# Optimization experiments

Measured on AMD Instinct MI355X. Metric: run time of the kernel, lower is better.

Reference implementation:

```python
import jax, jax.numpy as jnp
import numpy as np

B, T = 8192, 26
V, E, H, L = 23, 100, 128, 64  # vocab, emb dim, GRU hidden, latent; LSTM hidden = E


def setup_inputs() -> dict:
    key = jax.random.key(0)
    ks = jax.random.split(key, 16)
    rn = lambda k, shape, scale=0.1: (jax.random.normal(k, shape, jnp.float32) * scale)
    emb = rn(ks[0], (V, E)).at[0].set(0.0)  # padding_idx=0 row zeroed
    return {
        "z": jax.random.normal(ks[1], (B, L), jnp.float32),
        "x_in": jax.random.randint(ks[2], (B, T), 0, V),
        "emb": emb,
        "fc_z_w": rn(ks[3], (H, L)), "fc_z_b": rn(ks[4], (H,)),
        "gru_wih": rn(ks[5], (3 * H, E)), "gru_whh": rn(ks[6], (3 * H, H)),
        "gru_bih": rn(ks[7], (3 * H,)), "gru_bhh": rn(ks[8], (3 * H,)),
        "lstm_wih": rn(ks[9], (4 * E, H)), "lstm_whh": rn(ks[10], (4 * E, E)),
        "lstm_bih": rn(ks[11], (4 * E,)), "lstm_bhh": rn(ks[12], (4 * E,)),
        "out_w": rn(ks[13], (V, E)), "out_b": rn(ks[14], (V,)),
    }


def _gru(e, h0, Wih, Whh, bih, bhh):
    # e: (B,T,E); precompute input projections for all steps, scan over T.
    xg = jnp.einsum('bti,gi->btg', e, Wih) + bih  # (B,T,3H)

    def step(h, x):
        hg = h @ Whh.T + bhh
        xr, xz, xn = jnp.split(x, 3, axis=-1)
        hr, hz, hn = jnp.split(hg, 3, axis=-1)
        r = jax.nn.sigmoid(xr + hr)
        zg = jax.nn.sigmoid(xz + hz)
        n = jnp.tanh(xn + r * hn)
        h_new = (1.0 - zg) * n + zg * h
        return h_new, h_new

    _, ys = jax.lax.scan(step, h0, jnp.swapaxes(xg, 0, 1))  # (T,B,H)
    return jnp.swapaxes(ys, 0, 1)


def _lstm(x, h0, c0, Wih, Whh, bih, bhh):
    xg = jnp.einsum('bti,gi->btg', x, Wih) + bih  # (B,T,4E)

    def step(hc, xt):
        h, c = hc
        g = xt + h @ Whh.T + bhh
        i, f, gg, o = jnp.split(g, 4, axis=-1)
        c_new = jax.nn.sigmoid(f) * c + jax.nn.sigmoid(i) * jnp.tanh(gg)
        h_new = jax.nn.sigmoid(o) * jnp.tanh(c_new)
        return (h_new, c_new), h_new

    _, ys = jax.lax.scan(step, (h0, c0), jnp.swapaxes(xg, 0, 1))
    return jnp.swapaxes(ys, 0, 1)


def reference(z, x_in, emb, fc_z_w, fc_z_b, gru_wih, gru_whh, gru_bih, gru_bhh,
              lstm_wih, lstm_whh, lstm_bih, lstm_bhh, out_w, out_b):
    h0 = jnp.tanh(z @ fc_z_w.T + fc_z_b)            # (B,H)
    e = emb[x_in]                                    # (B,T,E)
    y = _gru(e, h0, gru_wih, gru_whh, gru_bih, gru_bhh)           # (B,T,H)
    zeros = jnp.zeros((z.shape[0], E), dtype=z.dtype)
    y = _lstm(y, zeros, zeros, lstm_wih, lstm_whh, lstm_bih, lstm_bhh)  # (B,T,E)
    logits = jnp.einsum('bte,ve->btv', y, out_w) + out_b          # (B,T,V)
    return logits
```

## Files before the change

kernel.cpp:

```cpp
#include <hip/hip_runtime.h>
#include <stdint.h>
#include <stddef.h>

#define BB 8192
#define TT 26
#define VV 23
#define EE 100
#define HH 128
#define LL 64

typedef __attribute__((ext_vector_type(8))) short bf16x8;
typedef __attribute__((ext_vector_type(4))) float f32x4;

#define MFMA(a, b, c) __builtin_amdgcn_mfma_f32_16x16x32_bf16((a), (b), (c), 0, 0, 0)

#define OFF_GRUW   0ull
#define OFF_TBL    98304ull
#define OFF_LSTMW  122880ull
#define OFF_OUTW   352256ull
#define OFF_FCZW   360448ull
#define OFF_LBIAS  376832ull

#define L_LW    0
#define L_HF    114688
#define L_LH    131072
#define L_IDX   147456
#define L_TOTAL 148480

__device__ __forceinline__ void force_frag(bf16x8& v) { asm volatile("" : "+v"(v)); }

__device__ __forceinline__ unsigned short f2bf(float f) {
  union { float f; unsigned u; } v; v.f = f;
  unsigned u = v.u;
  return (unsigned short)((u + 0x7FFFu + ((u >> 16) & 1u)) >> 16);
}
__device__ __forceinline__ unsigned short f2bf_fast(float f) {
  union { float f; unsigned u; } v; v.f = f;
  return (unsigned short)((v.u + 0x8000u) >> 16);
}
#define LOG2E 1.4426950408889634f
__device__ __forceinline__ float sigm(float x) {
  return __builtin_amdgcn_rcpf(1.0f + __builtin_amdgcn_exp2f(-x * LOG2E));
}
__device__ __forceinline__ float tanh_(float x) {
  return __builtin_fmaf(-2.0f,
      __builtin_amdgcn_rcpf(1.0f + __builtin_amdgcn_exp2f(x * (2.0f * LOG2E))), 1.0f);
}

__global__ __launch_bounds__(512) void prep_table_kernel(
    const float* __restrict__ emb, const float* __restrict__ gru_wih,
    const float* __restrict__ gru_bih, char* __restrict__ ws)
{
  __shared__ float emb_s[VV * EE];
  __shared__ float wih_s[16 * EE];
  __shared__ float bih_s[16];
  const int tid = threadIdx.x;
  const int ct  = blockIdx.x;
  const int n0  = ct * 16;

  for (int i = tid; i < VV * EE; i += 512) emb_s[i] = emb[i];
  for (int i = tid; i < 16 * EE; i += 512) wih_s[i] = gru_wih[n0 * EE + i];
  if (tid < 16) bih_s[tid] = gru_bih[n0 + tid];
  __syncthreads();

  const int j    = tid & 7;
  const int lane = (tid >> 3) & 63;
  const int n16  = lane & 15;
  const int k    = ((lane >> 4) & 3) * 8 + j;
  float v = 0.0f;
  if (k < VV) {
    const float* ep = emb_s + k * EE;
    const float* wp = wih_s + n16 * EE;
    float s0 = 0.f, s1 = 0.f, s2 = 0.f, s3 = 0.f;
#pragma unroll 5
    for (int m = 0; m < EE; m += 4) {
      s0 += ep[m] * wp[m];         s1 += ep[m + 1] * wp[m + 1];
      s2 += ep[m + 2] * wp[m + 2]; s3 += ep[m + 3] * wp[m + 3];
    }
    v = bih_s[n16] + ((s0 + s1) + (s2 + s3));
  }
  *(unsigned short*)(ws + OFF_TBL + (size_t)(ct * 512 + tid) * 2) = f2bf(v);
}

__global__ __launch_bounds__(256) void prep_main_kernel(
    const float* __restrict__ fc_z_w, const float* __restrict__ gru_whh,
    const float* __restrict__ lstm_wih, const float* __restrict__ lstm_whh,
    const float* __restrict__ lstm_bih, const float* __restrict__ lstm_bhh,
    const float* __restrict__ out_w, char* __restrict__ ws)
{
  int e = blockIdx.x * 256 + threadIdx.x;

  if (e < 49152) {
    int j = e & 7, lane = (e >> 3) & 63, kc = (e >> 9) & 3, ct = e >> 11;
    int n = ct * 16 + (lane & 15);
    int k = kc * 32 + ((lane >> 4) & 3) * 8 + j;
    *(unsigned short*)(ws + OFF_GRUW + (size_t)e * 2) = f2bf(gru_whh[n * HH + k]);
    return;
  }
  e -= 49152;
  if (e < 114688) {
    int j = e & 7, lane = (e >> 3) & 63, kc = (e >> 9) & 7, ct = e >> 12;
    int row = ct * 16 + (lane & 15);
    int g = row / 112, c = row % 112;
    int q = (lane >> 4) & 3;
    float v = 0.0f;
    if (c < EE) {
      if (kc < 4) {
        int k = kc * 32 + q * 8 + j;
        v = lstm_wih[(g * EE + c) * HH + k];
      } else {
        int k = (kc - 4) * 32 + q * 8 + j;
        if (k < EE) v = lstm_whh[(g * EE + c) * EE + k];
      }
    }
    *(unsigned short*)(ws + OFF_LSTMW + (size_t)e * 2) = f2bf(v);
    return;
  }
  e -= 114688;
  if (e < 4096) {
    int j = e & 7, lane = (e >> 3) & 63, kc = (e >> 9) & 3, ct = e >> 11;
    int n = ct * 16 + (lane & 15);
    int k = kc * 32 + ((lane >> 4) & 3) * 8 + j;
    float v = (n < VV && k < EE) ? out_w[n * EE + k] : 0.0f;
    *(unsigned short*)(ws + OFF_OUTW + (size_t)e * 2) = f2bf(v);
    return;
  }
  e -= 4096;
  if (e < 8192) {
    int j = e & 7, lane = (e >> 3) & 63, kc = (e >> 9) & 1, ct = e >> 10;
    int n = ct * 16 + (lane & 15);
    int k = kc * 32 + ((lane >> 4) & 3) * 8 + j;
    *(unsigned short*)(ws + OFF_FCZW + (size_t)e * 2) = f2bf(fc_z_w[n * LL + k]);
    return;
  }
  e -= 8192;
  if (e < 448) {
    int g = e / 112, c = e % 112;
    float v = (c < EE) ? (lstm_bih[g * EE + c] + lstm_bhh[g * EE + c]) : 0.0f;
    *(float*)(ws + OFF_LBIAS + (size_t)e * 4) = v;
  }
}

__global__ __launch_bounds__(1024, 4) void fused_kernel(
    const float* __restrict__ z, const int* __restrict__ x_in,
    const float* __restrict__ fc_z_b, const float* __restrict__ gru_bhh,
    const unsigned short* __restrict__ gruw, const unsigned short* __restrict__ tbl,
    const unsigned short* __restrict__ fczw,
    const unsigned short* __restrict__ lstmw, const float* __restrict__ lbias,
    const float* __restrict__ out_b, const unsigned short* __restrict__ outw,
    float* __restrict__ out)
{
  extern __shared__ char smem[];
  unsigned short* lwlds = (unsigned short*)(smem + L_LW);
  char*           hfrag = smem + L_HF;
  char*           lhbuf = smem + L_LH;
  unsigned char*  idx_lds = (unsigned char*)(smem + L_IDX);

  const int tid  = threadIdx.x;
  const int wv   = tid >> 6;
  const int lane = tid & 63;
  const int l15  = lane & 15;
  const int q    = (lane >> 4) & 3;
  const int blk  = blockIdx.x;

  for (int i = tid; i < 8192; i += 1024)
    ((unsigned short*)lhbuf)[i] = 0;
  for (int f = tid; f < 7168; f += 1024) {
    int frag_i = f >> 6, within = f & 63;
    int ct = frag_i >> 2, kcl = frag_i & 3;
    *(bf16x8*)((char*)lwlds + (size_t)frag_i * 1024 + within * 16) =
        *(const bf16x8*)(lstmw + ((size_t)(ct * 8 + 4 + kcl)) * 512 + within * 8);
  }

  if (wv < 8) {
    {
      int rid = wv * 64 + lane;
      for (int i = rid; i < TT * 32; i += 512) {
        int t = i >> 5, r = i & 31;
        idx_lds[i] = (unsigned char)x_in[(blk * 32 + r) * TT + t];
      }
    }
    bf16x8 gw[3][4], tw[3];
#pragma unroll
    for (int g = 0; g < 3; g++) {
      int ct = g * 8 + wv;
#pragma unroll
      for (int kc = 0; kc < 4; kc++) {
        gw[g][kc] = *(const bf16x8*)(gruw + (size_t)(ct * 4 + kc) * 512 + lane * 8);
        force_frag(gw[g][kc]);
      }
      tw[g] = *(const bf16x8*)(tbl + (size_t)ct * 512 + lane * 8);
      force_frag(tw[g]);
    }
    const int col = wv * 16 + l15;
    const float b_r = gru_bhh[0 * HH + col];
    const float b_z = gru_bhh[1 * HH + col];
    const float b_n = gru_bhh[2 * HH + col];
    const int wbase = (col >> 5) * 512 + ((col >> 3) & 3) * 128 + (col & 7);

    float h[2][4];
    {
      bf16x8 fw0 = *(const bf16x8*)(fczw + (size_t)(wv * 2 + 0) * 512 + lane * 8);
      bf16x8 fw1 = *(const bf16x8*)(fczw + (size_t)(wv * 2 + 1) * 512 + lane * 8);
      float fzb = fc_z_b[col];
#pragma unroll
      for (int mt = 0; mt < 2; mt++) {
        const float* zp = z + (size_t)(blk * 32 + mt * 16 + l15) * LL + q * 8;
        f32x4 z0 = *(const f32x4*)(zp);
        f32x4 z1 = *(const f32x4*)(zp + 4);
        f32x4 z2 = *(const f32x4*)(zp + 32);
        f32x4 z3 = *(const f32x4*)(zp + 36);
        bf16x8 za0, za1;
#pragma unroll
        for (int j = 0; j < 4; j++) {
          za0[j]     = (short)f2bf(z0[j]);
          za0[4 + j] = (short)f2bf(z1[j]);
          za1[j]     = (short)f2bf(z2[j]);
          za1[4 + j] = (short)f2bf(z3[j]);
        }
        f32x4 acc = {fzb, fzb, fzb, fzb};
        acc = MFMA(za0, fw0, acc);
        acc = MFMA(za1, fw1, acc);
#pragma unroll
        for (int i = 0; i < 4; i++) {
          h[mt][i] = tanh_(acc[i]);
          ((unsigned short*)(hfrag + mt * 4096))[wbase + (q * 4 + i) * 8]
              = f2bf_fast(h[mt][i]);
        }
      }
    }
    __syncthreads();

    for (int p = 0; p < TT + 2; p++) {
      if (p < TT) {
#pragma unroll
        for (int mt = 0; mt < 2; mt++) {
          int iv = idx_lds[p * 32 + mt * 16 + l15];
          bf16x8 oh;
#pragma unroll
          for (int j = 0; j < 8; j++)
            oh[j] = (short)((iv == q * 8 + j) ? 0x3F80 : 0);

          f32x4 ar  = {b_r, b_r, b_r, b_r};
          f32x4 az  = {b_z, b_z, b_z, b_z};
          f32x4 ahn = {b_n, b_n, b_n, b_n};
          f32x4 axn = {0.0f, 0.0f, 0.0f, 0.0f};
          ar  = MFMA(oh, tw[0], ar);
          az  = MFMA(oh, tw[1], az);
          axn = MFMA(oh, tw[2], axn);

          bf16x8 a[4];
#pragma unroll
          for (int kc = 0; kc < 4; kc++)
            a[kc] = *(const bf16x8*)(hfrag + (p & 1) * 8192 + mt * 4096
                                     + kc * 1024 + lane * 16);
#pragma unroll
          for (int kc = 0; kc < 4; kc++) {
            ar  = MFMA(a[kc], gw[0][kc], ar);
            az  = MFMA(a[kc], gw[1][kc], az);
            ahn = MFMA(a[kc], gw[2][kc], ahn);
          }
#pragma unroll
          for (int i = 0; i < 4; i++) {
            float r  = sigm(ar[i]);
            float zg = sigm(az[i]);
            float n  = tanh_(__builtin_fmaf(r, ahn[i], axn[i]));
            h[mt][i] = __builtin_fmaf(zg, h[mt][i] - n, n);
            ((unsigned short*)(hfrag + ((p + 1) & 1) * 8192 + mt * 4096))
                [wbase + (q * 4 + i) * 8] = f2bf_fast(h[mt][i]);
          }
        }
      }
      __syncthreads();
    }
  } else if (wv < 15) {
    const int tile = wv - 8;
    bf16x8 lwy[4][4];
#pragma unroll
    for (int g = 0; g < 4; g++)
#pragma unroll
      for (int kc = 0; kc < 4; kc++) {
        lwy[g][kc] = *(const bf16x8*)(lstmw + (size_t)((g * 7 + tile) * 8 + kc) * 512 + lane * 8);
        force_frag(lwy[g][kc]);
      }
    const int col = tile * 16 + l15;
    float b[4];
#pragma unroll
    for (int g = 0; g < 4; g++) b[g] = lbias[g * 112 + col];
    const int wbase = (col >> 5) * 512 + ((col >> 3) & 3) * 128 + (col & 7);
    float c[2][4] = {{0, 0, 0, 0}, {0, 0, 0, 0}};
    __syncthreads();

    for (int p = 0; p < TT + 2; p++) {
      if (p >= 1 && p <= TT) {
#pragma unroll
        for (int mt = 0; mt < 2; mt++) {
          f32x4 ai = {b[0], b[0], b[0], b[0]};
          f32x4 af = {b[1], b[1], b[1], b[1]};
          f32x4 ag = {b[2], b[2], b[2], b[2]};
          f32x4 ao = {b[3], b[3], b[3], b[3]};
#pragma unroll
          for (int kc = 0; kc < 4; kc++) {
            bf16x8 ya = *(const bf16x8*)(hfrag + (p & 1) * 8192 + mt * 4096
                                         + kc * 1024 + lane * 16);
            ai = MFMA(ya, lwy[0][kc], ai);
            af = MFMA(ya, lwy[1][kc], af);
            ag = MFMA(ya, lwy[2][kc], ag);
            ao = MFMA(ya, lwy[3][kc], ao);
          }
#pragma unroll
          for (int kc = 0; kc < 4; kc++) {
            bf16x8 ha = *(const bf16x8*)(lhbuf + ((p - 1) & 1) * 8192 + mt * 4096
                                         + kc * 1024 + lane * 16);
            const char* wb = (const char*)lwlds + (size_t)(tile * 4 + kc) * 1024 + lane * 16;
            bf16x8 w0 = *(const bf16x8*)(wb);
            bf16x8 w1 = *(const bf16x8*)(wb + 28672);
            bf16x8 w2 = *(const bf16x8*)(wb + 2 * 28672);
            bf16x8 w3 = *(const bf16x8*)(wb + 3 * 28672);
            ai = MFMA(ha, w0, ai);
            af = MFMA(ha, w1, af);
            ag = MFMA(ha, w2, ag);
            ao = MFMA(ha, w3, ao);
          }
#pragma unroll
          for (int i = 0; i < 4; i++) {
            float ii = sigm(ai[i]), ff = sigm(af[i]);
            float gg = tanh_(ag[i]), oo = sigm(ao[i]);
            float cn = __builtin_fmaf(ff, c[mt][i], ii * gg);
            c[mt][i] = cn;
            ((unsigned short*)(lhbuf + (p & 1) * 8192 + mt * 4096))
                [wbase + (q * 4 + i) * 8] = f2bf_fast(oo * tanh_(cn));
          }
        }
      }
      __syncthreads();
    }
  } else {
    bf16x8 ow[2][4];
#pragma unroll
    for (int ct = 0; ct < 2; ct++)
#pragma unroll
      for (int kc = 0; kc < 4; kc++) {
        ow[ct][kc] = *(const bf16x8*)(outw + (size_t)(ct * 4 + kc) * 512 + lane * 8);
        force_frag(ow[ct][kc]);
      }
    float ob[2];
#pragma unroll
    for (int ct = 0; ct < 2; ct++) {
      int cv = ct * 16 + l15;
      ob[ct] = (cv < VV) ? out_b[cv] : 0.0f;
    }
    __syncthreads();

    for (int p = 0; p < TT + 2; p++) {
      if (p >= 2) {
        const int t = p - 2;
#pragma unroll
        for (int mt = 0; mt < 2; mt++) {
          bf16x8 ha[4];
#pragma unroll
          for (int kc = 0; kc < 4; kc++)
            ha[kc] = *(const bf16x8*)(lhbuf + ((p - 1) & 1) * 8192 + mt * 4096
                                      + kc * 1024 + lane * 16);
#pragma unroll
          for (int ct = 0; ct < 2; ct++) {
            f32x4 acc = {ob[ct], ob[ct], ob[ct], ob[ct]};
#pragma unroll
            for (int kc = 0; kc < 4; kc++)
              acc = MFMA(ha[kc], ow[ct][kc], acc);
            int cv = ct * 16 + l15;
            if (cv < VV) {
#pragma unroll
              for (int i = 0; i < 4; i++) {
                int rowg = blk * 32 + mt * 16 + q * 4 + i;
                out[((size_t)rowg * TT + t) * VV + cv] = acc[i];
              }
            }
          }
        }
      }
      __syncthreads();
    }
  }
}

extern "C" void kernel_launch(void* const* d_in, const int* in_sizes, int n_in,
                              void* d_out, int out_size, void* d_ws, size_t ws_size,
                              hipStream_t stream) {
  (void)in_sizes; (void)n_in; (void)out_size; (void)ws_size;
  const float* z        = (const float*)d_in[0];
  const int*   x_in     = (const int*)  d_in[1];
  const float* emb      = (const float*)d_in[2];
  const float* fc_z_w   = (const float*)d_in[3];
  const float* fc_z_b   = (const float*)d_in[4];
  const float* gru_wih  = (const float*)d_in[5];
  const float* gru_whh  = (const float*)d_in[6];
  const float* gru_bih  = (const float*)d_in[7];
  const float* gru_bhh  = (const float*)d_in[8];
  const float* lstm_wih = (const float*)d_in[9];
  const float* lstm_whh = (const float*)d_in[10];
  const float* lstm_bih = (const float*)d_in[11];
  const float* lstm_bhh = (const float*)d_in[12];
  const float* out_w    = (const float*)d_in[13];
  const float* out_b    = (const float*)d_in[14];
  char*  ws  = (char*)d_ws;
  float* out = (float*)d_out;

  const unsigned short* gruw  = (const unsigned short*)(ws + OFF_GRUW);
  const unsigned short* tblp  = (const unsigned short*)(ws + OFF_TBL);
  const unsigned short* lstmw = (const unsigned short*)(ws + OFF_LSTMW);
  const unsigned short* outw  = (const unsigned short*)(ws + OFF_OUTW);
  const unsigned short* fczw  = (const unsigned short*)(ws + OFF_FCZW);
  const float*          lbias = (const float*)(ws + OFF_LBIAS);

  static int lds_attr_set = 0;
  (void)lds_attr_set;
  hipFuncSetAttribute((const void*)fused_kernel,
                      hipFuncAttributeMaxDynamicSharedMemorySize, L_TOTAL);

  prep_main_kernel<<<690, 256, 0, stream>>>(fc_z_w, gru_whh, lstm_wih, lstm_whh,
                                            lstm_bih, lstm_bhh, out_w, ws);
  prep_table_kernel<<<24, 512, 0, stream>>>(emb, gru_wih, gru_bih, ws);
  fused_kernel<<<256, 1024, L_TOTAL, stream>>>(z, x_in, fc_z_b, gru_bhh,
                                               gruw, tblp, fczw, lstmw, lbias,
                                               out_b, outw, out);
}
```

Baseline: 187.9 us.

## Merge prep kernels, fold GRU r/z biases into table, interleave LSTM MFMAs

The two weight-prep kernels become a single 738-block launch. This saves one kernel launch, and the GRU r/z hidden biases are pre-added into the embedding-projection table so the recurrent loop starts those accumulators at zero. In the LSTM warps, the fourth K-chunk of the input weights is reloaded from global each step instead of staying in registers, which cuts register pressure. Both M tiles are now computed together so each weight fragment is reused across two MFMAs and the independent MFMA chains interleave. The per-step global reload adds memory traffic inside the serial loop.

New measurement: 185.9 us. Within noise of the previous version (-1.1%).

```diff
diff --git a/kernel.cpp b/kernel.cpp
--- a/kernel.cpp
+++ b/kernel.cpp
@@ -47,48 +47,56 @@
       __builtin_amdgcn_rcpf(1.0f + __builtin_amdgcn_exp2f(x * (2.0f * LOG2E))), 1.0f);
 }
 
-__global__ __launch_bounds__(512) void prep_table_kernel(
+__global__ __launch_bounds__(256) void prep_kernel(
+    const float* __restrict__ fc_z_w, const float* __restrict__ gru_whh,
+    const float* __restrict__ lstm_wih, const float* __restrict__ lstm_whh,
+    const float* __restrict__ lstm_bih, const float* __restrict__ lstm_bhh,
+    const float* __restrict__ out_w,
     const float* __restrict__ emb, const float* __restrict__ gru_wih,
-    const float* __restrict__ gru_bih, char* __restrict__ ws)
+    const float* __restrict__ gru_bih, const float* __restrict__ gru_bhh,
+    char* __restrict__ ws)
 {
   __shared__ float emb_s[VV * EE];
   __shared__ float wih_s[16 * EE];
   __shared__ float bih_s[16];
+  const int blk = blockIdx.x;
   const int tid = threadIdx.x;
-  const int ct  = blockIdx.x;
-  const int n0  = ct * 16;
-
-  for (int i = tid; i < VV * EE; i += 512) emb_s[i] = emb[i];
-  for (int i = tid; i < 16 * EE; i += 512) wih_s[i] = gru_wih[n0 * EE + i];
-  if (tid < 16) bih_s[tid] = gru_bih[n0 + tid];
-  __syncthreads();
-
-  const int j    = tid & 7;
-  const int lane = (tid >> 3) & 63;
-  const int n16  = lane & 15;
-  const int k    = ((lane >> 4) & 3) * 8 + j;
-  float v = 0.0f;
-  if (k < VV) {
-    const float* ep = emb_s + k * EE;
-    const float* wp = wih_s + n16 * EE;
-    float s0 = 0.f, s1 = 0.f, s2 = 0.f, s3 = 0.f;
+
+  if (blk >= 690) {
+    const int blk2 = blk - 690;
+    const int ct   = blk2 >> 1;
+    const int half = blk2 & 1;
+    const int n0   = ct * 16;
+
+    for (int i = tid; i < VV * EE; i += 256) emb_s[i] = emb[i];
+    for (int i = tid; i < 16 * EE; i += 256) wih_s[i] = gru_wih[n0 * EE + i];
+    if (tid < 16) bih_s[tid] = gru_bih[n0 + tid];
+    __syncthreads();
+
+    const int t512 = half * 256 + tid;
+    const int j    = t512 & 7;
+    const int lane = (t512 >> 3) & 63;
+    const int n16  = lane & 15;
+    const int k    = ((lane >> 4) & 3) * 8 + j;
+    const int g    = ct >> 3;
+    float v = 0.0f;
+    if (k < VV) {
+      const float* ep = emb_s + k * EE;
+      const float* wp = wih_s + n16 * EE;
+      float s0 = 0.f, s1 = 0.f, s2 = 0.f, s3 = 0.f;
 #pragma unroll 5
-    for (int m = 0; m < EE; m += 4) {
-      s0 += ep[m] * wp[m];         s1 += ep[m + 1] * wp[m + 1];
-      s2 += ep[m + 2] * wp[m + 2]; s3 += ep[m + 3] * wp[m + 3];
-    }
-    v = bih_s[n16] + ((s0 + s1) + (s2 + s3));
-  }
-  *(unsigned short*)(ws + OFF_TBL + (size_t)(ct * 512 + tid) * 2) = f2bf(v);
-}
-
-__global__ __launch_bounds__(256) void prep_main_kernel(
-    const float* __restrict__ fc_z_w, const float* __restrict__ gru_whh,
-    const float* __restrict__ lstm_wih, const float* __restrict__ lstm_whh,
-    const float* __restrict__ lstm_bih, const float* __restrict__ lstm_bhh,
-    const float* __restrict__ out_w, char* __restrict__ ws)
-{
-  int e = blockIdx.x * 256 + threadIdx.x;
+      for (int m = 0; m < EE; m += 4) {
+        s0 += ep[m] * wp[m];         s1 += ep[m + 1] * wp[m + 1];
+        s2 += ep[m + 2] * wp[m + 2]; s3 += ep[m + 3] * wp[m + 3];
+      }
+      v = bih_s[n16] + ((s0 + s1) + (s2 + s3));
+      if (g < 2) v += gru_bhh[g * HH + (ct & 7) * 16 + n16];
+    }
+    *(unsigned short*)(ws + OFF_TBL + (size_t)(ct * 512 + t512) * 2) = f2bf(v);
+    return;
+  }
+
+  int e = blk * 256 + tid;
 
   if (e < 49152) {
     int j = e & 7, lane = (e >> 3) & 63, kc = (e >> 9) & 3, ct = e >> 11;
@@ -193,8 +201,6 @@
       force_frag(tw[g]);
     }
     const int col = wv * 16 + l15;
-    const float b_r = gru_bhh[0 * HH + col];
-    const float b_z = gru_bhh[1 * HH + col];
     const float b_n = gru_bhh[2 * HH + col];
     const int wbase = (col >> 5) * 512 + ((col >> 3) & 3) * 128 + (col & 7);
 
@@ -241,8 +247,8 @@
           for (int j = 0; j < 8; j++)
             oh[j] = (short)((iv == q * 8 + j) ? 0x3F80 : 0);
 
-          f32x4 ar  = {b_r, b_r, b_r, b_r};
-          f32x4 az  = {b_z, b_z, b_z, b_z};
+          f32x4 ar  = {0.0f, 0.0f, 0.0f, 0.0f};
+          f32x4 az  = {0.0f, 0.0f, 0.0f, 0.0f};
           f32x4 ahn = {b_n, b_n, b_n, b_n};
           f32x4 axn = {0.0f, 0.0f, 0.0f, 0.0f};
           ar  = MFMA(oh, tw[0], ar);
@@ -275,11 +281,11 @@
     }
   } else if (wv < 15) {
     const int tile = wv - 8;
-    bf16x8 lwy[4][4];
+    bf16x8 lwy[4][3];
 #pragma unroll
     for (int g = 0; g < 4; g++)
 #pragma unroll
-      for (int kc = 0; kc < 4; kc++) {
+      for (int kc = 0; kc < 3; kc++) {
         lwy[g][kc] = *(const bf16x8*)(lstmw + (size_t)((g * 7 + tile) * 8 + kc) * 512 + lane * 8);
         force_frag(lwy[g][kc]);
       }
@@ -293,39 +299,69 @@
 
     for (int p = 0; p < TT + 2; p++) {
       if (p >= 1 && p <= TT) {
+        bf16x8 yw3[4];
+#pragma unroll
+        for (int g = 0; g < 4; g++)
+          yw3[g] = *(const bf16x8*)(lstmw + (size_t)((g * 7 + tile) * 8 + 3) * 512 + lane * 8);
+
+        f32x4 acc[2][4];
+#pragma unroll
+        for (int mt = 0; mt < 2; mt++)
+#pragma unroll
+          for (int g = 0; g < 4; g++) {
+            f32x4 ini = {b[g], b[g], b[g], b[g]};
+            acc[mt][g] = ini;
+          }
+
+#pragma unroll
+        for (int kc = 0; kc < 3; kc++) {
+          bf16x8 ya0 = *(const bf16x8*)(hfrag + (p & 1) * 8192 + 0 * 4096
+                                        + kc * 1024 + lane * 16);
+          bf16x8 ya1 = *(const bf16x8*)(hfrag + (p & 1) * 8192 + 1 * 4096
+                                        + kc * 1024 + lane * 16);
+#pragma unroll
+          for (int g = 0; g < 4; g++) {
+            acc[0][g] = MFMA(ya0, lwy[g][kc], acc[0][g]);
+            acc[1][g] = MFMA(ya1, lwy[g][kc], acc[1][g]);
+          }
+        }
+        {
+          bf16x8 ya0 = *(const bf16x8*)(hfrag + (p & 1) * 8192 + 0 * 4096
+                                        + 3 * 1024 + lane * 16);
+          bf16x8 ya1 = *(const bf16x8*)(hfrag + (p & 1) * 8192 + 1 * 4096
+                                        + 3 * 1024 + lane * 16);
+#pragma unroll
+          for (int g = 0; g < 4; g++) {
+            acc[0][g] = MFMA(ya0, yw3[g], acc[0][g]);
+            acc[1][g] = MFMA(ya1, yw3[g], acc[1][g]);
+          }
+        }
+#pragma unroll
+        for (int kc = 0; kc < 4; kc++) {
+          const char* wb = (const char*)lwlds + (size_t)(tile * 4 + kc) * 1024 + lane * 16;
+          bf16x8 w0 = *(const bf16x8*)(wb);
+          bf16x8 w1 = *(const bf16x8*)(wb + 28672);
+          bf16x8 w2 = *(const bf16x8*)(wb + 2 * 28672);
+          bf16x8 w3 = *(const bf16x8*)(wb + 3 * 28672);
+          bf16x8 ha0 = *(const bf16x8*)(lhbuf + ((p - 1) & 1) * 8192 + 0 * 4096
+                                        + kc * 1024 + lane * 16);
+          bf16x8 ha1 = *(const bf16x8*)(lhbuf + ((p - 1) & 1) * 8192 + 1 * 4096
+                                        + kc * 1024 + lane * 16);
+          acc[0][0] = MFMA(ha0, w0, acc[0][0]);
+          acc[0][1] = MFMA(ha0, w1, acc[0][1]);
+          acc[0][2] = MFMA(ha0, w2, acc[0][2]);
+          acc[0][3] = MFMA(ha0, w3, acc[0][3]);
+          acc[1][0] = MFMA(ha1, w0, acc[1][0]);
+          acc[1][1] = MFMA(ha1, w1, acc[1][1]);
+          acc[1][2] = MFMA(ha1, w2, acc[1][2]);
+          acc[1][3] = MFMA(ha1, w3, acc[1][3]);
+        }
 #pragma unroll
         for (int mt = 0; mt < 2; mt++) {
-          f32x4 ai = {b[0], b[0], b[0], b[0]};
-          f32x4 af = {b[1], b[1], b[1], b[1]};
-          f32x4 ag = {b[2], b[2], b[2], b[2]};
-          f32x4 ao = {b[3], b[3], b[3], b[3]};
-#pragma unroll
-          for (int kc = 0; kc < 4; kc++) {
-            bf16x8 ya = *(const bf16x8*)(hfrag + (p & 1) * 8192 + mt * 4096
-                                         + kc * 1024 + lane * 16);
-            ai = MFMA(ya, lwy[0][kc], ai);
-            af = MFMA(ya, lwy[1][kc], af);
-            ag = MFMA(ya, lwy[2][kc], ag);
-            ao = MFMA(ya, lwy[3][kc], ao);
-          }
-#pragma unroll
-          for (int kc = 0; kc < 4; kc++) {
-            bf16x8 ha = *(const bf16x8*)(lhbuf + ((p - 1) & 1) * 8192 + mt * 4096
-                                         + kc * 1024 + lane * 16);
-            const char* wb = (const char*)lwlds + (size_t)(tile * 4 + kc) * 1024 + lane * 16;
-            bf16x8 w0 = *(const bf16x8*)(wb);
-            bf16x8 w1 = *(const bf16x8*)(wb + 28672);
-            bf16x8 w2 = *(const bf16x8*)(wb + 2 * 28672);
-            bf16x8 w3 = *(const bf16x8*)(wb + 3 * 28672);
-            ai = MFMA(ha, w0, ai);
-            af = MFMA(ha, w1, af);
-            ag = MFMA(ha, w2, ag);
-            ao = MFMA(ha, w3, ao);
-          }
 #pragma unroll
           for (int i = 0; i < 4; i++) {
-            float ii = sigm(ai[i]), ff = sigm(af[i]);
-            float gg = tanh_(ag[i]), oo = sigm(ao[i]);
+            float ii = sigm(acc[mt][0][i]), ff = sigm(acc[mt][1][i]);
+            float gg = tanh_(acc[mt][2][i]), oo = sigm(acc[mt][3][i]);
             float cn = __builtin_fmaf(ff, c[mt][i], ii * gg);
             c[mt][i] = cn;
             ((unsigned short*)(lhbuf + (p & 1) * 8192 + mt * 4096))
@@ -413,14 +449,12 @@
   const unsigned short* fczw  = (const unsigned short*)(ws + OFF_FCZW);
   const float*          lbias = (const float*)(ws + OFF_LBIAS);
 
-  static int lds_attr_set = 0;
-  (void)lds_attr_set;
   hipFuncSetAttribute((const void*)fused_kernel,
                       hipFuncAttributeMaxDynamicSharedMemorySize, L_TOTAL);
 
-  prep_main_kernel<<<690, 256, 0, stream>>>(fc_z_w, gru_whh, lstm_wih, lstm_whh,
-                                            lstm_bih, lstm_bhh, out_w, ws);
-  prep_table_kernel<<<24, 512, 0, stream>>>(emb, gru_wih, gru_bih, ws);
+  prep_kernel<<<738, 256, 0, stream>>>(fc_z_w, gru_whh, lstm_wih, lstm_whh,
+                                       lstm_bih, lstm_bhh, out_w,
+                                       emb, gru_wih, gru_bih, gru_bhh, ws);
   fused_kernel<<<256, 1024, L_TOTAL, stream>>>(z, x_in, fc_z_b, gru_bhh,
                                                gruw, tblp, fczw, lstmw, lbias,
                                                out_b, outw, out);
```
